# Kernel optimization log

Measured on AMD Instinct MI355X. Metric: run time of the kernel, lower is better.

The kernel has to match this reference:

```python
import jax, jax.numpy as jnp
import numpy as np

T, K, E, H, I = 1024, 2, 8, 2048, 768


def setup_inputs() -> dict:
    key = jax.random.key(0)
    k1, k2, k3, k4, k5 = jax.random.split(key, 5)
    hidden_states = jax.random.normal(k1, (T, H), dtype=jnp.float32)
    top_k_index = jax.random.randint(k2, (T, K), 0, E)
    logits = jax.random.normal(k3, (T, K), dtype=jnp.float32)
    top_k_weights = jax.nn.softmax(logits, axis=-1)  # realistic routing weights
    # Linear-style weights: gate_up [E, 2I, H], down [E, H, I]; scaled like trained params
    gate_up_proj = jax.random.normal(k4, (E, 2 * I, H), dtype=jnp.float32) * 0.02
    down_proj = jax.random.normal(k5, (E, H, I), dtype=jnp.float32) * 0.02
    return {
        "hidden_states": hidden_states,
        "top_k_index": top_k_index,
        "top_k_weights": top_k_weights,
        "gate_up_proj": gate_up_proj,
        "down_proj": down_proj,
    }


def reference(hidden_states, top_k_index, top_k_weights, gate_up_proj, down_proj):
    """Dense-dispatch MoE forward: same math as the per-expert 4-bit loop.

    For every token t and routed expert e (with routing weight w):
      gate, up = split(x_t @ Wgu_e^T); y_t += w * (silu(gate)*up) @ Wd_e^T
    Expressed densely over experts; non-routed (token, expert) pairs get a
    combine weight of 0, so they contribute nothing.
    """
    num_experts = gate_up_proj.shape[0]
    # combine[t, e] = sum_k w[t,k] * [top_k_index[t,k] == e]
    combine = jnp.sum(
        jax.nn.one_hot(top_k_index, num_experts, dtype=hidden_states.dtype)
        * top_k_weights[..., None],
        axis=1,
    )  # [T, E]
    # gate_up: [T, E, 2I]
    gu = jnp.einsum("th,eoh->teo", hidden_states, gate_up_proj)
    gate, up = jnp.split(gu, 2, axis=-1)
    h = jax.nn.silu(gate) * up  # [T, E, I]
    # fold combine weight in before the down projection (scalar per (t,e))
    h = h * combine[:, :, None]
    out = jnp.einsum("tei,ehi->th", h, down_proj)  # [T, H]
    return out.astype(hidden_states.dtype)
```

## Files before the change

### kernel.cpp

```cpp
#include <hip/hip_runtime.h>
#include <hip/hip_bf16.h>

#define T_TOK 1024
#define TOPK  2
#define NEXP  8
#define HDIM  2048
#define IDIM  768
#define MROW  384

typedef __attribute__((ext_vector_type(4))) float f32x4;
typedef __attribute__((ext_vector_type(4))) unsigned short u16x4;
typedef __attribute__((ext_vector_type(8))) short bf16x8;
typedef __attribute__((ext_vector_type(8))) unsigned short u16x8;
typedef __attribute__((ext_vector_type(8))) __bf16 bfv8;

__device__ __forceinline__ bf16x8 cvt8(f32x4 v0, f32x4 v1) {
  bfv8 r;
#pragma unroll
  for (int j = 0; j < 4; ++j) { r[j] = (__bf16)v0[j]; r[4 + j] = (__bf16)v1[j]; }
  return __builtin_bit_cast(bf16x8, r);
}

__device__ __forceinline__ void gload_lds16(const void* g, void* l) {
  __builtin_amdgcn_global_load_lds(
      (const __attribute__((address_space(1))) unsigned int*)((unsigned long long)g),
      (__attribute__((address_space(3))) unsigned int*)(unsigned int)(unsigned long long)(l),
      16, 0, 0);
}

#define GUP_OFF   17440832ull
#define GUP_HALF  (8ull * MROW * 1536)
#define WS_NEEDED (GUP_OFF + 2ull * GUP_HALF * 4ull)

__global__ void k_gather(const int* __restrict__ idx, const float* __restrict__ wts,
                         int* __restrict__ cnt, int* __restrict__ tok,
                         float* __restrict__ wl, int* __restrict__ inv) {
  int g = blockIdx.x * 256 + threadIdx.x;
  int e = idx[g];
  float w = wts[g];
  int pos = atomicAdd(&cnt[e], 1);
  if (pos < 2048) { tok[e * 2048 + pos] = g; wl[e * 2048 + pos] = w; }
  inv[g] = (pos < MROW) ? (e * MROW + pos) : -1;
}

__global__ __launch_bounds__(256) void k_compact(const float* __restrict__ x,
                                                 const int* __restrict__ inv,
                                                 unsigned short* __restrict__ xe) {
  int pid = blockIdx.x;
  int iv = inv[pid];
  if (iv < 0) return;
  const float* src = x + (size_t)(pid >> 1) * HDIM;
  unsigned short* dst = xe + (size_t)iv * HDIM;
  int i = threadIdx.x * 8;
  f32x4 a = *(const f32x4*)(src + i);
  f32x4 b = *(const f32x4*)(src + i + 4);
  *(bf16x8*)(dst + i) = cvt8(a, b);
}

__global__ __launch_bounds__(256) void k_gate_up_ks(
    const unsigned short* __restrict__ xe, const float* __restrict__ Wgu,
    const int* __restrict__ cnt, float* __restrict__ guP)
{
  const int b = blockIdx.x;
  const int e = b & 7;
  const int r = b >> 3;
  const int ks = r & 1;
  const int r2 = r >> 1;
  const int mt = r2 % 3;
  const int nb = r2 / 3;
  const int m0 = mt * 128;
  int cc = cnt[e]; if (cc > MROW) cc = MROW;
  if (m0 >= cc) return;
  const int col0 = nb * 32;
  const int kbase = ks * (HDIM / 2);

  __shared__ unsigned short sA[3 * 4096];
  __shared__ float          sB[3 * 2048];

  const int tid = threadIdx.x;
  const int lane = tid & 63, wid = tid >> 6;

  const unsigned short* xeE = xe + ((size_t)e * MROW + m0) * HDIM + kbase;
  const unsigned short* aSrc[2];
  unsigned int aDstOff[2];
#pragma unroll
  for (int i = 0; i < 2; ++i) {
    int row = wid * 32 + i * 16 + (lane >> 2);
    int csrc = (lane & 3) ^ (row & 3);
    aSrc[i] = xeE + (size_t)row * HDIM + csrc * 8;
    aDstOff[i] = (unsigned)(wid * 32 + i * 16) * 32;
  }

  const float* bSrc[2];
  unsigned int bDstOff[2];
#pragma unroll
  for (int i = 0; i < 2; ++i) {
    int row = wid * 16 + i * 8 + (lane >> 3);
    int c = lane & 7, h = c & 1, p = c >> 1;
    int psrc = p ^ (row & 3);
    int ocol = (row < 32) ? (col0 + row) : (IDIM + col0 + (row - 32));
    bSrc[i] = Wgu + ((size_t)e * 2 * IDIM + ocol) * HDIM + kbase + psrc * 8 + h * 4;
    bDstOff[i] = (unsigned)(wid * 16 + i * 8) * 32;
  }

  const int fl = lane & 15, q = lane >> 4;
  const int wm = (wid >> 1) * 64, wn = (wid & 1) * 16;

  f32x4 accg[4], accu[4];
#pragma unroll
  for (int rf = 0; rf < 4; ++rf) {
    accg[rf] = f32x4{0.f, 0.f, 0.f, 0.f};
    accu[rf] = f32x4{0.f, 0.f, 0.f, 0.f};
  }

  const int NS = (HDIM / 2) / 32;

  auto STAGE = [&](int step, int bo) {
    const int kt = step * 32;
#pragma unroll
    for (int i = 0; i < 2; ++i)
      gload_lds16(aSrc[i] + kt, &sA[bo * 4096 + aDstOff[i]]);
#pragma unroll
    for (int i = 0; i < 2; ++i)
      gload_lds16(bSrc[i] + kt, &sB[bo * 2048 + bDstOff[i]]);
  };

  auto COMPUTE = [&](int bo) {
    const unsigned short* A = sA + bo * 4096;
    const float* B = sB + bo * 2048;
    bf16x8 a[4];
#pragma unroll
    for (int rf = 0; rf < 4; ++rf) {
      int rr = wm + rf * 16 + fl;
      a[rf] = *(const bf16x8*)(A + rr * 32 + ((q ^ (rr & 3)) * 8));
    }
    bf16x8 g2, u2;
    {
      int rg = wn + fl;
      const float* pg = B + rg * 32 + ((q ^ (rg & 3)) * 8);
      g2 = cvt8(*(const f32x4*)pg, *(const f32x4*)(pg + 4));
      int ru = 32 + wn + fl;
      const float* pu = B + ru * 32 + ((q ^ (ru & 3)) * 8);
      u2 = cvt8(*(const f32x4*)pu, *(const f32x4*)(pu + 4));
    }
#pragma unroll
    for (int rf = 0; rf < 4; ++rf) {
      accg[rf] = __builtin_amdgcn_mfma_f32_16x16x32_bf16(a[rf], g2, accg[rf], 0, 0, 0);
      accu[rf] = __builtin_amdgcn_mfma_f32_16x16x32_bf16(a[rf], u2, accu[rf], 0, 0, 0);
    }
  };

  STAGE(0, 0);
  STAGE(1, 1);
  asm volatile("s_waitcnt vmcnt(4)" ::: "memory");
  __builtin_amdgcn_sched_barrier(0);
  __builtin_amdgcn_s_barrier();
  __builtin_amdgcn_sched_barrier(0);

  int oC = 0, oN = 1, oNN = 2;
#pragma unroll 1
  for (int i = 0; i < NS; ++i) {
    const bool st = (i + 2) < NS;
    if (st) STAGE(i + 2, oNN);
    COMPUTE(oC);
    if (i < NS - 1) {
      if (st) { asm volatile("s_waitcnt vmcnt(4)" ::: "memory"); }
      else    { asm volatile("s_waitcnt vmcnt(0)" ::: "memory"); }
      __builtin_amdgcn_sched_barrier(0);
      __builtin_amdgcn_s_barrier();
      __builtin_amdgcn_sched_barrier(0);
    }
    int t = oC; oC = oN; oN = oNN; oNN = t;
  }

  float* guE = guP + (size_t)ks * GUP_HALF + ((size_t)e * MROW) * 1536;
  const int q4 = q * 4;
#pragma unroll
  for (int rf = 0; rf < 4; ++rf)
#pragma unroll
    for (int v = 0; v < 4; ++v) {
      int rowl = wm + rf * 16 + q4 + v;
      if (m0 + rowl < cc) {
        size_t base = (size_t)(m0 + rowl) * 1536 + col0 + wn + fl;
        guE[base]       = accg[rf][v];
        guE[base + 768] = accu[rf][v];
      }
    }
}

__global__ __launch_bounds__(256) void k_silu_ep(
    const float* __restrict__ guP, const int* __restrict__ cnt,
    const float* __restrict__ wl, unsigned short* __restrict__ hb)
{
  int id = blockIdx.x * 256 + threadIdx.x;
  int e = id / (MROW * 192);
  int rem = id % (MROW * 192);
  int row = rem / 192;
  int c4 = (rem % 192) * 4;
  int cc = cnt[e]; if (cc > MROW) cc = MROW;
  if (row >= cc) return;

  size_t base = ((size_t)e * MROW + row) * 1536 + c4;
  f32x4 g = *(const f32x4*)(guP + base) + *(const f32x4*)(guP + GUP_HALF + base);
  f32x4 u = *(const f32x4*)(guP + base + 768) + *(const f32x4*)(guP + GUP_HALF + base + 768);
  float w = wl[e * 2048 + row];

  u16x4 o;
#pragma unroll
  for (int j = 0; j < 4; ++j) {
    float s = g[j] / (1.f + __expf(-g[j]));
    o[j] = __builtin_bit_cast(unsigned short, (__bf16)(s * u[j] * w));
  }
  *(u16x4*)(hb + ((size_t)e * MROW + row) * IDIM + c4) = o;
}

__global__ __launch_bounds__(256) void k_gate_up(
    const unsigned short* __restrict__ xe, const float* __restrict__ Wgu,
    const int* __restrict__ cnt, const float* __restrict__ wl,
    unsigned short* __restrict__ hb)
{
  const int b = blockIdx.x;
  const int e = b & 7;
  const int r = b >> 3;
  const int mt = r % 3;
  const int nb = r / 3;
  const int m0 = mt * 128;
  int cc = cnt[e]; if (cc > MROW) cc = MROW;
  if (m0 >= cc) return;
  const int col0 = nb * 32;

  __shared__ unsigned short sA[3 * 4096];
  __shared__ float          sB[3 * 2048];
  __shared__ float sW[128];

  const int tid = threadIdx.x;
  const int lane = tid & 63, wid = tid >> 6;

  if (tid < 128) sW[tid] = (m0 + tid < cc) ? wl[e * 2048 + m0 + tid] : 0.f;

  const unsigned short* xeE = xe + ((size_t)e * MROW + m0) * HDIM;
  const unsigned short* aSrc[2];
  unsigned int aDstOff[2];
#pragma unroll
  for (int i = 0; i < 2; ++i) {
    int row = wid * 32 + i * 16 + (lane >> 2);
    int csrc = (lane & 3) ^ (row & 3);
    aSrc[i] = xeE + (size_t)row * HDIM + csrc * 8;
    aDstOff[i] = (unsigned)(wid * 32 + i * 16) * 32;
  }

  const float* bSrc[2];
  unsigned int bDstOff[2];
#pragma unroll
  for (int i = 0; i < 2; ++i) {
    int row = wid * 16 + i * 8 + (lane >> 3);
    int c = lane & 7, h = c & 1, p = c >> 1;
    int psrc = p ^ (row & 3);
    int ocol = (row < 32) ? (col0 + row) : (IDIM + col0 + (row - 32));
    bSrc[i] = Wgu + ((size_t)e * 2 * IDIM + ocol) * HDIM + psrc * 8 + h * 4;
    bDstOff[i] = (unsigned)(wid * 16 + i * 8) * 32;
  }

  const int fl = lane & 15, q = lane >> 4;
  const int wm = (wid >> 1) * 64, wn = (wid & 1) * 16;

  f32x4 accg[4], accu[4];
#pragma unroll
  for (int rf = 0; rf < 4; ++rf) {
    accg[rf] = f32x4{0.f, 0.f, 0.f, 0.f};
    accu[rf] = f32x4{0.f, 0.f, 0.f, 0.f};
  }

  const int NS = HDIM / 32;

  auto STAGE = [&](int step, int bo) {
    const int kt = step * 32;
#pragma unroll
    for (int i = 0; i < 2; ++i)
      gload_lds16(aSrc[i] + kt, &sA[bo * 4096 + aDstOff[i]]);
#pragma unroll
    for (int i = 0; i < 2; ++i)
      gload_lds16(bSrc[i] + kt, &sB[bo * 2048 + bDstOff[i]]);
  };

  auto COMPUTE = [&](int bo) {
    const unsigned short* A = sA + bo * 4096;
    const float* B = sB + bo * 2048;
    bf16x8 a[4];
#pragma unroll
    for (int rf = 0; rf < 4; ++rf) {
      int rr = wm + rf * 16 + fl;
      a[rf] = *(const bf16x8*)(A + rr * 32 + ((q ^ (rr & 3)) * 8));
    }
    bf16x8 g2, u2;
    {
      int rg = wn + fl;
      const float* pg = B + rg * 32 + ((q ^ (rg & 3)) * 8);
      g2 = cvt8(*(const f32x4*)pg, *(const f32x4*)(pg + 4));
      int ru = 32 + wn + fl;
      const float* pu = B + ru * 32 + ((q ^ (ru & 3)) * 8);
      u2 = cvt8(*(const f32x4*)pu, *(const f32x4*)(pu + 4));
    }
#pragma unroll
    for (int rf = 0; rf < 4; ++rf) {
      accg[rf] = __builtin_amdgcn_mfma_f32_16x16x32_bf16(a[rf], g2, accg[rf], 0, 0, 0);
      accu[rf] = __builtin_amdgcn_mfma_f32_16x16x32_bf16(a[rf], u2, accu[rf], 0, 0, 0);
    }
  };

  STAGE(0, 0);
  STAGE(1, 1);
  asm volatile("s_waitcnt vmcnt(4)" ::: "memory");
  __builtin_amdgcn_sched_barrier(0);
  __builtin_amdgcn_s_barrier();
  __builtin_amdgcn_sched_barrier(0);

  int oC = 0, oN = 1, oNN = 2;
#pragma unroll 1
  for (int i = 0; i < NS; ++i) {
    const bool st = (i + 2) < NS;
    if (st) STAGE(i + 2, oNN);
    COMPUTE(oC);
    if (i < NS - 1) {
      if (st) { asm volatile("s_waitcnt vmcnt(4)" ::: "memory"); }
      else    { asm volatile("s_waitcnt vmcnt(0)" ::: "memory"); }
      __builtin_amdgcn_sched_barrier(0);
      __builtin_amdgcn_s_barrier();
      __builtin_amdgcn_sched_barrier(0);
    }
    int t = oC; oC = oN; oN = oNN; oNN = t;
  }

  unsigned short* hbE = hb + (size_t)e * MROW * IDIM;
  const int q4 = q * 4;
#pragma unroll
  for (int rf = 0; rf < 4; ++rf)
#pragma unroll
    for (int v = 0; v < 4; ++v) {
      int rowl = wm + rf * 16 + q4 + v;
      if (m0 + rowl < cc) {
        float g = accg[rf][v], u = accu[rf][v];
        float s = g / (1.f + __expf(-g));
        float h = s * u * sW[rowl];
        hbE[(size_t)(m0 + rowl) * IDIM + col0 + wn + fl] =
            __builtin_bit_cast(unsigned short, (__bf16)h);
      }
    }
}

__global__ __launch_bounds__(256, 3) void k_down(
    const unsigned short* __restrict__ hb, const float* __restrict__ Wd,
    const int* __restrict__ cnt, const int* __restrict__ tok,
    float* __restrict__ out)
{
  const int b = blockIdx.x;
  const int e = b & 7;
  const int r = b >> 3;
  const int mt = r % 6;
  const int nb = r / 6;
  const int m0 = mt * 64;
  int cc = cnt[e]; if (cc > MROW) cc = MROW;
  if (m0 >= cc) return;
  const int col0 = nb * 64;

  __shared__ unsigned short sA[3 * 4096];
  __shared__ unsigned short sB[3 * 4096];
  __shared__ int sTok[64];

  const int tid = threadIdx.x;
  const int lane = tid & 63, wid = tid >> 6;
  if (tid < 64) sTok[tid] = (m0 + tid < cc) ? (tok[e * 2048 + m0 + tid] >> 1) : 0;

  const unsigned short* hbE = hb + ((size_t)e * MROW + m0) * IDIM;
  const unsigned short* aSrc[2];
  unsigned int aDstOff[2];
#pragma unroll
  for (int i = 0; i < 2; ++i) {
    int row = wid * 16 + i * 8 + (lane >> 3);
    int csrc = (lane & 7) ^ (row & 7);
    aSrc[i] = hbE + (size_t)row * IDIM + csrc * 8;
    aDstOff[i] = (unsigned)(wid * 16 + i * 8) * 64;
  }

  const int brow = tid >> 2, cq = (tid & 3);
  const float* bSrc = Wd + ((size_t)e * HDIM + col0 + brow) * IDIM + cq * 16;
  unsigned int bDst[2];
#pragma unroll
  for (int c2 = 0; c2 < 2; ++c2)
    bDst[c2] = (unsigned)(brow * 64 + (((cq * 2 + c2) ^ (brow & 7)) * 8));

  const int fl = lane & 15, q = lane >> 4;
  const int wm = (wid >> 1) * 32, wn = (wid & 1) * 32;

  f32x4 acc[2][2];
#pragma unroll
  for (int mf = 0; mf < 2; ++mf)
#pragma unroll
    for (int nf = 0; nf < 2; ++nf) acc[mf][nf] = f32x4{0.f, 0.f, 0.f, 0.f};

  f32x4 blA[4], blB[4];
  const int NS = IDIM / 64;

  auto COMPUTE = [&](int bo) {
    const unsigned short* A = sA + bo;
    const unsigned short* B = sB + bo;
#pragma unroll
    for (int s = 0; s < 2; ++s) {
      bf16x8 a[2], bb[2];
#pragma unroll
      for (int mf = 0; mf < 2; ++mf) {
        int rr = wm + mf * 16 + fl;
        a[mf] = *(const bf16x8*)(A + rr * 64 + (((s * 4 + q) ^ (rr & 7)) * 8));
      }
#pragma unroll
      for (int nf = 0; nf < 2; ++nf) {
        int rn = wn + nf * 16 + fl;
        bb[nf] = *(const bf16x8*)(B + rn * 64 + (((s * 4 + q) ^ (rn & 7)) * 8));
      }
#pragma unroll
      for (int mf = 0; mf < 2; ++mf)
#pragma unroll
        for (int nf = 0; nf < 2; ++nf)
          acc[mf][nf] = __builtin_amdgcn_mfma_f32_16x16x32_bf16(a[mf], bb[nf], acc[mf][nf], 0, 0, 0);
    }
  };

  auto ITER = [&](int ks, f32x4 (&blR)[4], f32x4 (&blW)[4],
                  int oC, int oN, int oNN) {
    const bool nL = (ks + 2) < NS;
    const bool nW = (ks + 1) < NS;
    if (nL) {
#pragma unroll
      for (int i = 0; i < 2; ++i)
        gload_lds16(aSrc[i] + (ks + 2) * 64, &sA[oNN + aDstOff[i]]);
#pragma unroll
      for (int j = 0; j < 4; ++j)
        blW[j] = *(const f32x4*)(bSrc + (ks + 2) * 64 + j * 4);
    }
    if (nW) {
#pragma unroll
      for (int c2 = 0; c2 < 2; ++c2)
        *(bf16x8*)&sB[oN + bDst[c2]] = cvt8(blR[c2 * 2], blR[c2 * 2 + 1]);
    }
    COMPUTE(oC);
    if (nW) {
      if (nL) { asm volatile("s_waitcnt vmcnt(6) lgkmcnt(0)" ::: "memory"); }
      else    { asm volatile("s_waitcnt vmcnt(0) lgkmcnt(0)" ::: "memory"); }
      __builtin_amdgcn_sched_barrier(0);
      __builtin_amdgcn_s_barrier();
      __builtin_amdgcn_sched_barrier(0);
    }
  };

#pragma unroll
  for (int i = 0; i < 2; ++i) gload_lds16(aSrc[i], &sA[aDstOff[i]]);
#pragma unroll
  for (int j = 0; j < 4; ++j) blA[j] = *(const f32x4*)(bSrc + j * 4);
#pragma unroll
  for (int i = 0; i < 2; ++i) gload_lds16(aSrc[i] + 64, &sA[4096 + aDstOff[i]]);
#pragma unroll
  for (int j = 0; j < 4; ++j) blB[j] = *(const f32x4*)(bSrc + 64 + j * 4);
#pragma unroll
  for (int c2 = 0; c2 < 2; ++c2)
    *(bf16x8*)&sB[bDst[c2]] = cvt8(blA[c2 * 2], blA[c2 * 2 + 1]);
  asm volatile("s_waitcnt vmcnt(6) lgkmcnt(0)" ::: "memory");
  __builtin_amdgcn_sched_barrier(0);
  __builtin_amdgcn_s_barrier();
  __builtin_amdgcn_sched_barrier(0);

  int oC = 0, oN = 4096, oNN = 8192;
  for (int ks = 0; ks < NS; ks += 2) {
    ITER(ks, blB, blA, oC, oN, oNN);
    int t = oC; oC = oN; oN = oNN; oNN = t;
    ITER(ks + 1, blA, blB, oC, oN, oNN);
    t = oC; oC = oN; oN = oNN; oNN = t;
  }

  const int q4 = q * 4;
#pragma unroll
  for (int mf = 0; mf < 2; ++mf)
#pragma unroll
    for (int nf = 0; nf < 2; ++nf)
#pragma unroll
      for (int v = 0; v < 4; ++v) {
        int rowl = wm + mf * 16 + q4 + v;
        if (m0 + rowl < cc) {
          int t = sTok[rowl];
          atomicAdd(out + (size_t)t * HDIM + col0 + wn + nf * 16 + fl, acc[mf][nf][v]);
        }
      }
}

extern "C" void kernel_launch(void* const* d_in, const int* in_sizes, int n_in,
                              void* d_out, int out_size, void* d_ws, size_t ws_size,
                              hipStream_t stream) {
  const float* x   = (const float*)d_in[0];
  const int*   idx = (const int*)d_in[1];
  const float* wts = (const float*)d_in[2];
  const float* Wgu = (const float*)d_in[3];
  const float* Wd  = (const float*)d_in[4];
  float* out = (float*)d_out;

  char* ws = (char*)d_ws;
  int*            cnt = (int*)(ws + 0);
  int*            tok = (int*)(ws + 64);
  float*          wl  = (float*)(ws + 65600);
  int*            inv = (int*)(ws + 131136);
  unsigned short* xe  = (unsigned short*)(ws + 139328);
  unsigned short* hb  = (unsigned short*)(ws + 12722240);
  float*          guP = (float*)(ws + GUP_OFF);

  hipMemsetAsync(cnt, 0, NEXP * sizeof(int), stream);
  hipMemsetAsync(out, 0, (size_t)T_TOK * HDIM * sizeof(float), stream);
  k_gather<<<dim3((T_TOK * TOPK) / 256), 256, 0, stream>>>(idx, wts, cnt, tok, wl, inv);
  k_compact<<<dim3(T_TOK * TOPK), 256, 0, stream>>>(x, inv, xe);

  if (ws_size >= WS_NEEDED) {
    k_gate_up_ks<<<dim3(NEXP * 3 * 24 * 2), 256, 0, stream>>>(xe, Wgu, cnt, guP);
    k_silu_ep<<<dim3(NEXP * MROW * 192 / 256), 256, 0, stream>>>(guP, cnt, wl, hb);
  } else {
    k_gate_up<<<dim3(NEXP * 3 * 24), 256, 0, stream>>>(xe, Wgu, cnt, wl, hb);
  }
  k_down<<<dim3(NEXP * 6 * 32), 256, 0, stream>>>(hb, Wd, cnt, tok, out);
}
```

Measured before the change: 105.5 us.

## Halve gate-up N tile, double grid, switch to double-buffered LDS pipeline

The split-K gate/up kernel now computes 16 output columns per block instead of 32, so the grid doubles to 2304 blocks. Each wave takes 32 rows with a single N fragment. The three-stage LDS ring with manual vmcnt waits becomes a simpler two-buffer ping-pong using __syncthreads, and the B swizzle moves to an 8-way XOR on float4 chunks. The goal is more parallelism and lower LDS use per block, at the cost of loading the A tile twice as often overall, more MFMA-idle time per barrier, and less prefetch depth.

```diff
diff --git a/kernel.cpp b/kernel.cpp
--- a/kernel.cpp
+++ b/kernel.cpp
@@ -71,11 +71,11 @@
   const int m0 = mt * 128;
   int cc = cnt[e]; if (cc > MROW) cc = MROW;
   if (m0 >= cc) return;
-  const int col0 = nb * 32;
+  const int col0 = nb * 16;
   const int kbase = ks * (HDIM / 2);
 
-  __shared__ unsigned short sA[3 * 4096];
-  __shared__ float          sB[3 * 2048];
+  __shared__ unsigned short sA[2][128 * 32];
+  __shared__ float          sB[2][32 * 32];
 
   const int tid = threadIdx.x;
   const int lane = tid & 63, wid = tid >> 6;
@@ -91,24 +91,23 @@
     aDstOff[i] = (unsigned)(wid * 32 + i * 16) * 32;
   }
 
-  const float* bSrc[2];
-  unsigned int bDstOff[2];
-#pragma unroll
-  for (int i = 0; i < 2; ++i) {
-    int row = wid * 16 + i * 8 + (lane >> 3);
-    int c = lane & 7, h = c & 1, p = c >> 1;
-    int psrc = p ^ (row & 3);
-    int ocol = (row < 32) ? (col0 + row) : (IDIM + col0 + (row - 32));
-    bSrc[i] = Wgu + ((size_t)e * 2 * IDIM + ocol) * HDIM + kbase + psrc * 8 + h * 4;
-    bDstOff[i] = (unsigned)(wid * 16 + i * 8) * 32;
+  const float* bSrc;
+  unsigned int bDstOff;
+  {
+    int row = wid * 8 + (lane >> 3);
+    int c = lane & 7;
+    int csrc = c ^ (row & 7);
+    int ocol = (row < 16) ? (col0 + row) : (IDIM + col0 + (row - 16));
+    bSrc = Wgu + ((size_t)e * 2 * IDIM + ocol) * HDIM + kbase + csrc * 4;
+    bDstOff = (unsigned)(wid * 8) * 32;
   }
 
   const int fl = lane & 15, q = lane >> 4;
-  const int wm = (wid >> 1) * 64, wn = (wid & 1) * 16;
-
-  f32x4 accg[4], accu[4];
-#pragma unroll
-  for (int rf = 0; rf < 4; ++rf) {
+  const int wm = wid * 32;
+
+  f32x4 accg[2], accu[2];
+#pragma unroll
+  for (int rf = 0; rf < 2; ++rf) {
     accg[rf] = f32x4{0.f, 0.f, 0.f, 0.f};
     accu[rf] = f32x4{0.f, 0.f, 0.f, 0.f};
   }
@@ -119,69 +118,57 @@
     const int kt = step * 32;
 #pragma unroll
     for (int i = 0; i < 2; ++i)
-      gload_lds16(aSrc[i] + kt, &sA[bo * 4096 + aDstOff[i]]);
-#pragma unroll
-    for (int i = 0; i < 2; ++i)
-      gload_lds16(bSrc[i] + kt, &sB[bo * 2048 + bDstOff[i]]);
+      gload_lds16(aSrc[i] + kt, &sA[bo][aDstOff[i]]);
+    gload_lds16(bSrc + kt, &sB[bo][bDstOff]);
   };
 
   auto COMPUTE = [&](int bo) {
-    const unsigned short* A = sA + bo * 4096;
-    const float* B = sB + bo * 2048;
-    bf16x8 a[4];
-#pragma unroll
-    for (int rf = 0; rf < 4; ++rf) {
+    const unsigned short* A = sA[bo];
+    const float* B = sB[bo];
+    bf16x8 a[2];
+#pragma unroll
+    for (int rf = 0; rf < 2; ++rf) {
       int rr = wm + rf * 16 + fl;
       a[rf] = *(const bf16x8*)(A + rr * 32 + ((q ^ (rr & 3)) * 8));
     }
     bf16x8 g2, u2;
     {
-      int rg = wn + fl;
-      const float* pg = B + rg * 32 + ((q ^ (rg & 3)) * 8);
-      g2 = cvt8(*(const f32x4*)pg, *(const f32x4*)(pg + 4));
-      int ru = 32 + wn + fl;
-      const float* pu = B + ru * 32 + ((q ^ (ru & 3)) * 8);
-      u2 = cvt8(*(const f32x4*)pu, *(const f32x4*)(pu + 4));
-    }
-#pragma unroll
-    for (int rf = 0; rf < 4; ++rf) {
+      int rg = fl;
+      f32x4 g0 = *(const f32x4*)(B + rg * 32 + (((2 * q)     ^ (rg & 7)) * 4));
+      f32x4 g1 = *(const f32x4*)(B + rg * 32 + (((2 * q + 1) ^ (rg & 7)) * 4));
+      g2 = cvt8(g0, g1);
+      int ru = 16 + fl;
+      f32x4 u0 = *(const f32x4*)(B + ru * 32 + (((2 * q)     ^ (ru & 7)) * 4));
+      f32x4 u1 = *(const f32x4*)(B + ru * 32 + (((2 * q + 1) ^ (ru & 7)) * 4));
+      u2 = cvt8(u0, u1);
+    }
+#pragma unroll
+    for (int rf = 0; rf < 2; ++rf) {
       accg[rf] = __builtin_amdgcn_mfma_f32_16x16x32_bf16(a[rf], g2, accg[rf], 0, 0, 0);
       accu[rf] = __builtin_amdgcn_mfma_f32_16x16x32_bf16(a[rf], u2, accu[rf], 0, 0, 0);
     }
   };
 
   STAGE(0, 0);
-  STAGE(1, 1);
-  asm volatile("s_waitcnt vmcnt(4)" ::: "memory");
-  __builtin_amdgcn_sched_barrier(0);
-  __builtin_amdgcn_s_barrier();
-  __builtin_amdgcn_sched_barrier(0);
-
-  int oC = 0, oN = 1, oNN = 2;
+  __syncthreads();
+  int buf = 0;
 #pragma unroll 1
   for (int i = 0; i < NS; ++i) {
-    const bool st = (i + 2) < NS;
-    if (st) STAGE(i + 2, oNN);
-    COMPUTE(oC);
-    if (i < NS - 1) {
-      if (st) { asm volatile("s_waitcnt vmcnt(4)" ::: "memory"); }
-      else    { asm volatile("s_waitcnt vmcnt(0)" ::: "memory"); }
-      __builtin_amdgcn_sched_barrier(0);
-      __builtin_amdgcn_s_barrier();
-      __builtin_amdgcn_sched_barrier(0);
-    }
-    int t = oC; oC = oN; oN = oNN; oNN = t;
+    if (i + 1 < NS) STAGE(i + 1, buf ^ 1);
+    COMPUTE(buf);
+    __syncthreads();
+    buf ^= 1;
   }
 
   float* guE = guP + (size_t)ks * GUP_HALF + ((size_t)e * MROW) * 1536;
   const int q4 = q * 4;
 #pragma unroll
-  for (int rf = 0; rf < 4; ++rf)
+  for (int rf = 0; rf < 2; ++rf)
 #pragma unroll
     for (int v = 0; v < 4; ++v) {
       int rowl = wm + rf * 16 + q4 + v;
       if (m0 + rowl < cc) {
-        size_t base = (size_t)(m0 + rowl) * 1536 + col0 + wn + fl;
+        size_t base = (size_t)(m0 + rowl) * 1536 + col0 + fl;
         guE[base]       = accg[rf][v];
         guE[base + 768] = accu[rf][v];
       }
@@ -516,7 +503,7 @@
   k_compact<<<dim3(T_TOK * TOPK), 256, 0, stream>>>(x, inv, xe);
 
   if (ws_size >= WS_NEEDED) {
-    k_gate_up_ks<<<dim3(NEXP * 3 * 24 * 2), 256, 0, stream>>>(xe, Wgu, cnt, guP);
+    k_gate_up_ks<<<dim3(NEXP * 3 * 48 * 2), 256, 0, stream>>>(xe, Wgu, cnt, guP);
     k_silu_ep<<<dim3(NEXP * MROW * 192 / 256), 256, 0, stream>>>(guP, cnt, wl, hb);
   } else {
     k_gate_up<<<dim3(NEXP * 3 * 24), 256, 0, stream>>>(xe, Wgu, cnt, wl, hb);
```

After: 119.9 us. +13.6%, slower.

## Pre-convert gate_up weights to bf16 and fuse SiLU epilogue into GEMM

Applied to the files above, without the earlier changes.

Adds a kernel that converts the fp32 gate_up weights to bf16 in workspace on every call. The gate_up GEMM then loads bf16 tiles with 64-wide K steps and 64-row M tiles, with no split-K. The SiLU, up-multiply and routing-weight scaling are fused into the GEMM epilogue, which removes the fp32 partial-sum buffer and the separate SiLU kernel. The trade is an extra full read and write of the weight tensor in the conversion pass, in exchange for halving the bytes the GEMM reads for B and dropping the per-step in-loop conversion.

```diff
diff --git a/kernel.cpp b/kernel.cpp
--- a/kernel.cpp
+++ b/kernel.cpp
@@ -9,7 +9,6 @@
 #define MROW  384
 
 typedef __attribute__((ext_vector_type(4))) float f32x4;
-typedef __attribute__((ext_vector_type(4))) unsigned short u16x4;
 typedef __attribute__((ext_vector_type(8))) short bf16x8;
 typedef __attribute__((ext_vector_type(8))) unsigned short u16x8;
 typedef __attribute__((ext_vector_type(8))) __bf16 bfv8;
@@ -28,9 +27,8 @@
       16, 0, 0);
 }
 
-#define GUP_OFF   17440832ull
-#define GUP_HALF  (8ull * MROW * 1536)
-#define WS_NEEDED (GUP_OFF + 2ull * GUP_HALF * 4ull)
+#define WGB_OFF   17440832ull
+#define WS_NEEDED (WGB_OFF + 8ull * 1536 * 2048 * 2)
 
 __global__ void k_gather(const int* __restrict__ idx, const float* __restrict__ wts,
                          int* __restrict__ cnt, int* __restrict__ tok,
@@ -57,96 +55,103 @@
   *(bf16x8*)(dst + i) = cvt8(a, b);
 }
 
-__global__ __launch_bounds__(256) void k_gate_up_ks(
-    const unsigned short* __restrict__ xe, const float* __restrict__ Wgu,
-    const int* __restrict__ cnt, float* __restrict__ guP)
+__global__ __launch_bounds__(256) void k_wcvt(const float* __restrict__ Wgu,
+                                              unsigned short* __restrict__ wgb) {
+  size_t i = ((size_t)blockIdx.x * 256 + threadIdx.x) * 8;
+  f32x4 a = *(const f32x4*)(Wgu + i);
+  f32x4 b = *(const f32x4*)(Wgu + i + 4);
+  *(bf16x8*)(wgb + i) = cvt8(a, b);
+}
+
+__global__ __launch_bounds__(256, 3) void k_gate_up_gu(
+    const unsigned short* __restrict__ xe, const unsigned short* __restrict__ wgb,
+    const int* __restrict__ cnt, const float* __restrict__ wl,
+    unsigned short* __restrict__ hb)
 {
   const int b = blockIdx.x;
   const int e = b & 7;
   const int r = b >> 3;
-  const int ks = r & 1;
-  const int r2 = r >> 1;
-  const int mt = r2 % 3;
-  const int nb = r2 / 3;
-  const int m0 = mt * 128;
+  const int mt = r % 6;
+  const int nb = r / 6;
+  const int m0 = mt * 64;
   int cc = cnt[e]; if (cc > MROW) cc = MROW;
   if (m0 >= cc) return;
   const int col0 = nb * 32;
-  const int kbase = ks * (HDIM / 2);
 
   __shared__ unsigned short sA[3 * 4096];
-  __shared__ float          sB[3 * 2048];
+  __shared__ unsigned short sB[3 * 4096];
+  __shared__ float sW[64];
 
   const int tid = threadIdx.x;
   const int lane = tid & 63, wid = tid >> 6;
-
-  const unsigned short* xeE = xe + ((size_t)e * MROW + m0) * HDIM + kbase;
+  if (tid < 64) sW[tid] = (m0 + tid < cc) ? wl[e * 2048 + m0 + tid] : 0.f;
+
+  const unsigned short* xeE = xe + ((size_t)e * MROW + m0) * HDIM;
   const unsigned short* aSrc[2];
   unsigned int aDstOff[2];
 #pragma unroll
   for (int i = 0; i < 2; ++i) {
-    int row = wid * 32 + i * 16 + (lane >> 2);
-    int csrc = (lane & 3) ^ (row & 3);
+    int row = wid * 16 + i * 8 + (lane >> 3);
+    int csrc = (lane & 7) ^ (row & 7);
     aSrc[i] = xeE + (size_t)row * HDIM + csrc * 8;
-    aDstOff[i] = (unsigned)(wid * 32 + i * 16) * 32;
-  }
-
-  const float* bSrc[2];
+    aDstOff[i] = (unsigned)(wid * 16 + i * 8) * 64;
+  }
+
+  const unsigned short* bSrc[2];
   unsigned int bDstOff[2];
 #pragma unroll
   for (int i = 0; i < 2; ++i) {
     int row = wid * 16 + i * 8 + (lane >> 3);
-    int c = lane & 7, h = c & 1, p = c >> 1;
-    int psrc = p ^ (row & 3);
+    int csrc = (lane & 7) ^ (row & 7);
     int ocol = (row < 32) ? (col0 + row) : (IDIM + col0 + (row - 32));
-    bSrc[i] = Wgu + ((size_t)e * 2 * IDIM + ocol) * HDIM + kbase + psrc * 8 + h * 4;
-    bDstOff[i] = (unsigned)(wid * 16 + i * 8) * 32;
+    bSrc[i] = wgb + ((size_t)e * 2 * IDIM + ocol) * HDIM + csrc * 8;
+    bDstOff[i] = (unsigned)(wid * 16 + i * 8) * 64;
   }
 
   const int fl = lane & 15, q = lane >> 4;
-  const int wm = (wid >> 1) * 64, wn = (wid & 1) * 16;
-
-  f32x4 accg[4], accu[4];
-#pragma unroll
-  for (int rf = 0; rf < 4; ++rf) {
-    accg[rf] = f32x4{0.f, 0.f, 0.f, 0.f};
-    accu[rf] = f32x4{0.f, 0.f, 0.f, 0.f};
-  }
-
-  const int NS = (HDIM / 2) / 32;
-
-  auto STAGE = [&](int step, int bo) {
-    const int kt = step * 32;
+  const int wm = (wid >> 1) * 32, wn = (wid & 1) * 16;
+
+  f32x4 accg[2], accu[2];
+#pragma unroll
+  for (int mf = 0; mf < 2; ++mf) {
+    accg[mf] = f32x4{0.f, 0.f, 0.f, 0.f};
+    accu[mf] = f32x4{0.f, 0.f, 0.f, 0.f};
+  }
+
+  const int NS = HDIM / 64;
+
+  auto STAGE = [&](int ks, int bo) {
+    const int kt = ks * 64;
 #pragma unroll
     for (int i = 0; i < 2; ++i)
       gload_lds16(aSrc[i] + kt, &sA[bo * 4096 + aDstOff[i]]);
 #pragma unroll
     for (int i = 0; i < 2; ++i)
-      gload_lds16(bSrc[i] + kt, &sB[bo * 2048 + bDstOff[i]]);
+      gload_lds16(bSrc[i] + kt, &sB[bo * 4096 + bDstOff[i]]);
   };
 
   auto COMPUTE = [&](int bo) {
     const unsigned short* A = sA + bo * 4096;
-    const float* B = sB + bo * 2048;
-    bf16x8 a[4];
-#pragma unroll
-    for (int rf = 0; rf < 4; ++rf) {
-      int rr = wm + rf * 16 + fl;
-      a[rf] = *(const bf16x8*)(A + rr * 32 + ((q ^ (rr & 3)) * 8));
-    }
-    bf16x8 g2, u2;
-    {
-      int rg = wn + fl;
-      const float* pg = B + rg * 32 + ((q ^ (rg & 3)) * 8);
-      g2 = cvt8(*(const f32x4*)pg, *(const f32x4*)(pg + 4));
-      int ru = 32 + wn + fl;
-      const float* pu = B + ru * 32 + ((q ^ (ru & 3)) * 8);
-      u2 = cvt8(*(const f32x4*)pu, *(const f32x4*)(pu + 4));
-    }
-#pragma unroll
-    for (int rf = 0; rf < 4; ++rf) {
-      accg[rf] = __builtin_amdgcn_mfma_f32_16x16x32_bf16(a[rf], g2, accg[rf], 0, 0, 0);
-      accu[rf] = __builtin_amdgcn_mfma_f32_16x16x32_bf16(a[rf], u2, accu[rf], 0, 0, 0);
+    const unsigned short* B = sB + bo * 4096;
+#pragma unroll
+    for (int s = 0; s < 2; ++s) {
+      bf16x8 a[2], g2, u2;
+#pragma unroll
+      for (int mf = 0; mf < 2; ++mf) {
+        int rr = wm + mf * 16 + fl;
+        a[mf] = *(const bf16x8*)(A + rr * 64 + (((s * 4 + q) ^ (rr & 7)) * 8));
+      }
+      {
+        int rg = wn + fl;
+        g2 = *(const bf16x8*)(B + rg * 64 + (((s * 4 + q) ^ (rg & 7)) * 8));
+        int ru = 32 + wn + fl;
+        u2 = *(const bf16x8*)(B + ru * 64 + (((s * 4 + q) ^ (ru & 7)) * 8));
+      }
+#pragma unroll
+      for (int mf = 0; mf < 2; ++mf) {
+        accg[mf] = __builtin_amdgcn_mfma_f32_16x16x32_bf16(a[mf], g2, accg[mf], 0, 0, 0);
+        accu[mf] = __builtin_amdgcn_mfma_f32_16x16x32_bf16(a[mf], u2, accu[mf], 0, 0, 0);
+      }
     }
   };
 
@@ -173,45 +178,21 @@
     int t = oC; oC = oN; oN = oNN; oNN = t;
   }
 
-  float* guE = guP + (size_t)ks * GUP_HALF + ((size_t)e * MROW) * 1536;
+  unsigned short* hbE = hb + (size_t)e * MROW * IDIM;
   const int q4 = q * 4;
 #pragma unroll
-  for (int rf = 0; rf < 4; ++rf)
+  for (int mf = 0; mf < 2; ++mf)
 #pragma unroll
     for (int v = 0; v < 4; ++v) {
-      int rowl = wm + rf * 16 + q4 + v;
+      int rowl = wm + mf * 16 + q4 + v;
       if (m0 + rowl < cc) {
-        size_t base = (size_t)(m0 + rowl) * 1536 + col0 + wn + fl;
-        guE[base]       = accg[rf][v];
-        guE[base + 768] = accu[rf][v];
-      }
-    }
-}
-
-__global__ __launch_bounds__(256) void k_silu_ep(
-    const float* __restrict__ guP, const int* __restrict__ cnt,
-    const float* __restrict__ wl, unsigned short* __restrict__ hb)
-{
-  int id = blockIdx.x * 256 + threadIdx.x;
-  int e = id / (MROW * 192);
-  int rem = id % (MROW * 192);
-  int row = rem / 192;
-  int c4 = (rem % 192) * 4;
-  int cc = cnt[e]; if (cc > MROW) cc = MROW;
-  if (row >= cc) return;
-
-  size_t base = ((size_t)e * MROW + row) * 1536 + c4;
-  f32x4 g = *(const f32x4*)(guP + base) + *(const f32x4*)(guP + GUP_HALF + base);
-  f32x4 u = *(const f32x4*)(guP + base + 768) + *(const f32x4*)(guP + GUP_HALF + base + 768);
-  float w = wl[e * 2048 + row];
-
-  u16x4 o;
-#pragma unroll
-  for (int j = 0; j < 4; ++j) {
-    float s = g[j] / (1.f + __expf(-g[j]));
-    o[j] = __builtin_bit_cast(unsigned short, (__bf16)(s * u[j] * w));
-  }
-  *(u16x4*)(hb + ((size_t)e * MROW + row) * IDIM + c4) = o;
+        float g = accg[mf][v], u = accu[mf][v];
+        float s = g / (1.f + __expf(-g));
+        float h = s * u * sW[rowl];
+        hbE[(size_t)(m0 + rowl) * IDIM + col0 + wn + fl] =
+            __builtin_bit_cast(unsigned short, (__bf16)h);
+      }
+    }
 }
 
 __global__ __launch_bounds__(256) void k_gate_up(
@@ -508,7 +489,7 @@
   int*            inv = (int*)(ws + 131136);
   unsigned short* xe  = (unsigned short*)(ws + 139328);
   unsigned short* hb  = (unsigned short*)(ws + 12722240);
-  float*          guP = (float*)(ws + GUP_OFF);
+  unsigned short* wgb = (unsigned short*)(ws + WGB_OFF);
 
   hipMemsetAsync(cnt, 0, NEXP * sizeof(int), stream);
   hipMemsetAsync(out, 0, (size_t)T_TOK * HDIM * sizeof(float), stream);
@@ -516,8 +497,8 @@
   k_compact<<<dim3(T_TOK * TOPK), 256, 0, stream>>>(x, inv, xe);
 
   if (ws_size >= WS_NEEDED) {
-    k_gate_up_ks<<<dim3(NEXP * 3 * 24 * 2), 256, 0, stream>>>(xe, Wgu, cnt, guP);
-    k_silu_ep<<<dim3(NEXP * MROW * 192 / 256), 256, 0, stream>>>(guP, cnt, wl, hb);
+    k_wcvt<<<dim3((NEXP * 2 * IDIM * HDIM / 8) / 256), 256, 0, stream>>>(Wgu, wgb);
+    k_gate_up_gu<<<dim3(NEXP * 6 * 24), 256, 0, stream>>>(xe, wgb, cnt, wl, hb);
   } else {
     k_gate_up<<<dim3(NEXP * 3 * 24), 256, 0, stream>>>(xe, Wgu, cnt, wl, hb);
   }
```

Measured after the change: 121.0 us. 1.15x slower.
